# Performance work log

Measured on AMD Instinct MI355X. Metric: run time of the kernel, lower is better.

Reference implementation:

```python
import jax, jax.numpy as jnp
import numpy as np

B, C, H, W = 32, 3, 512, 512
OUT = (64, 64)  # (out_grid[0]=Nx, out_grid[1]=Ny)
SMALL = 1e-4


def setup_inputs() -> dict:
    key = jax.random.key(0)
    k1, k2 = jax.random.split(key, 2)
    X = jax.random.normal(k1, (B, C, H, W), dtype=jnp.float32)
    fan_in = C * H * W
    # localization net: flatten + dense(5); scaled so p ~ N(0,1) and exp(p) is stable
    W_loc = jax.random.normal(k2, (fan_in, 5), dtype=jnp.float32) / np.float32(np.sqrt(fan_in))
    b_loc = jnp.zeros((5,), dtype=jnp.float32)
    return {"X": X, "W_loc": W_loc, "b_loc": b_loc}


def reference(X, W_loc, b_loc):
    Bn = X.shape[0]
    # locnet: p = flatten(X) @ W_loc + b_loc  -> [B, 5]
    p = X.reshape(Bn, -1) @ W_loc + b_loc

    N = min(OUT)
    gx = OUT[0] * (p[:, 0] + 1.0) / 2.0          # [B]
    gy = OUT[1] * (p[:, 1] + 1.0) / 2.0          # [B]
    sigma2 = jnp.exp(p[:, 2])                    # [B]
    delta = jnp.exp(p[:, 3]) * (max(W, H) - 1) / (N - 1.0)  # [B]
    gamma = jnp.exp(p[:, 4])                     # [B]

    i1 = jnp.arange(OUT[0], dtype=jnp.float32)   # [Nx]
    i2 = jnp.arange(OUT[1], dtype=jnp.float32)   # [Ny]
    a = jnp.arange(W, dtype=jnp.float32)         # [W]
    b = jnp.arange(H, dtype=jnp.float32)         # [H]

    mx = gx[:, None] + delta[:, None] * (i1 - N / 2.0 - 0.5)  # [B, Nx]
    my = gy[:, None] + delta[:, None] * (i2 - N / 2.0 - 0.5)  # [B, Ny]

    Fx = jnp.exp(-((a - mx[:, :, None]) ** 2) / (2.0 * sigma2[:, None, None]))  # [B,Nx,W]
    Fx = Fx / (Fx.sum(axis=-1, keepdims=True) + SMALL)
    Fy = jnp.exp(-((b - my[:, :, None]) ** 2) / (2.0 * sigma2[:, None, None]))  # [B,Ny,H]
    Fy = Fy / (Fy.sum(axis=-1, keepdims=True) + SMALL)

    # glimpse read: gamma * Fy @ X @ Fx^T, done as batched contractions
    Fyx = jnp.einsum('bnh,bchw->bcnw', Fy, X)        # [B,C,Ny,W]
    out = jnp.einsum('bcnw,bmw->bcnm', Fyx, Fx)      # [B,C,Ny,Nx]
    return gamma[:, None, None, None] * out
```

## Files before the change

### kernel.cpp

```cpp
#include <hip/hip_runtime.h>
#include <math.h>

#define B_ 32
#define C_ 3
#define H_ 512
#define W_ 512
#define NOUT 64
#define FAN (C_*H_*W_)

#define CHUNKS 384
#define CELEMS (FAN / CHUNKS)
#define BGROUPS 4

#define P_OFF 0
#define FX_OFF 256
#define FY_OFF (FX_OFF + B_*NOUT*W_)

typedef __bf16 bf16x8 __attribute__((ext_vector_type(8)));
typedef float f32x4 __attribute__((ext_vector_type(4)));

__device__ __forceinline__ unsigned short f2bf(float f) {
    unsigned int u = __float_as_uint(f);
    u = (u + 0x7FFFu + ((u >> 16) & 1u)) >> 16;
    return (unsigned short)u;
}
__device__ __forceinline__ float bf2f(unsigned short h) {
    return __uint_as_float(((unsigned int)h) << 16);
}

__global__ __launch_bounds__(256) void k_locnet(const float* __restrict__ X,
                                                const float* __restrict__ Wl,
                                                float* __restrict__ ws) {
    const int chunk = blockIdx.x;
    const int b0 = blockIdx.y * 8;
    const int t = threadIdx.x;

    float acc[8][5] = {};
    const size_t base = (size_t)chunk * CELEMS;

    for (int k = t; k < CELEMS / 4; k += 256) {
        const size_t i0 = base + (size_t)k * 4;
        const float4* W4 = (const float4*)(Wl + i0 * 5);
        float4 w0 = W4[0], w1 = W4[1], w2 = W4[2], w3 = W4[3], w4 = W4[4];
        float wv[20] = {w0.x, w0.y, w0.z, w0.w,
                        w1.x, w1.y, w1.z, w1.w,
                        w2.x, w2.y, w2.z, w2.w,
                        w3.x, w3.y, w3.z, w3.w,
                        w4.x, w4.y, w4.z, w4.w};
        #pragma unroll
        for (int bb = 0; bb < 8; bb++) {
            float4 x = *(const float4*)(X + (size_t)(b0 + bb) * FAN + i0);
            float xv[4] = {x.x, x.y, x.z, x.w};
            #pragma unroll
            for (int e = 0; e < 4; e++)
                #pragma unroll
                for (int j = 0; j < 5; j++)
                    acc[bb][j] += xv[e] * wv[e * 5 + j];
        }
    }

    #pragma unroll
    for (int off = 32; off > 0; off >>= 1)
        #pragma unroll
        for (int bb = 0; bb < 8; bb++)
            #pragma unroll
            for (int j = 0; j < 5; j++)
                acc[bb][j] += __shfl_down(acc[bb][j], off);

    __shared__ float sred[4][40];
    const int wave = t >> 6, lane = t & 63;
    if (lane == 0) {
        #pragma unroll
        for (int bb = 0; bb < 8; bb++)
            #pragma unroll
            for (int j = 0; j < 5; j++)
                sred[wave][bb * 5 + j] = acc[bb][j];
    }
    __syncthreads();
    if (t < 40) {
        float s = sred[0][t] + sred[1][t] + sred[2][t] + sred[3][t];
        atomicAdd(&ws[P_OFF + b0 * 5 + t], s);
    }
}

__global__ __launch_bounds__(256) void k_filters(const float* __restrict__ bl,
                                                 float* __restrict__ ws) {
    const int n = blockIdx.x;
    const int b = blockIdx.y;
    const int which = blockIdx.z;
    const int t = threadIdx.x;

    const float p0 = ws[P_OFF + b * 5 + 0] + bl[0];
    const float p1 = ws[P_OFF + b * 5 + 1] + bl[1];
    const float p2 = ws[P_OFF + b * 5 + 2] + bl[2];
    const float p3 = ws[P_OFF + b * 5 + 3] + bl[3];

    const float g = (which == 0) ? 32.f * (p0 + 1.f) : 32.f * (p1 + 1.f);
    const float sigma2 = expf(p2);
    const float inv2s = 0.5f / sigma2;
    const float delta = expf(p3) * (511.0f / 63.0f);
    const float mean = g + delta * ((float)n - 32.5f);

    float d0 = (float)t - mean;
    float f0 = expf(-d0 * d0 * inv2s);
    float d1 = (float)(t + 256) - mean;
    float f1 = expf(-d1 * d1 * inv2s);

    float s = f0 + f1;
    #pragma unroll
    for (int off = 32; off > 0; off >>= 1) s += __shfl_down(s, off);
    __shared__ float sred[4];
    __shared__ float stot;
    const int wave = t >> 6, lane = t & 63;
    if (lane == 0) sred[wave] = s;
    __syncthreads();
    if (t == 0) stot = sred[0] + sred[1] + sred[2] + sred[3] + 1e-4f;
    __syncthreads();
    const float scale = 1.0f / stot;

    float* dst = ws + (which == 0 ? FX_OFF : FY_OFF) + ((size_t)b * NOUT + n) * W_;
    dst[t] = f0 * scale;
    dst[t + 256] = f1 * scale;
}

#define KC 64
#define PITCH 72
#define TSZ (64 * PITCH)

__global__ __launch_bounds__(256) void k_glimpse(const float* __restrict__ X,
                                                 const float* __restrict__ bl,
                                                 const float* __restrict__ ws,
                                                 float* __restrict__ out) {
    const int hc = blockIdx.x;
    const int bc = blockIdx.y;
    const int b = bc / 3;
    const int t = threadIdx.x;
    const int lane = t & 63;
    const int wv = t >> 6;
    const int l15 = lane & 15;
    const int quad = lane >> 4;
    const int hbase = hc * 64;

    __shared__ __align__(16) unsigned short lds[4 * TSZ];
    unsigned short* Xh = lds;
    unsigned short* Xl = lds + TSZ;
    unsigned short* Fh = lds + 2 * TSZ;
    unsigned short* Fl = lds + 3 * TSZ;

    const float* Xp  = X + (size_t)bc * (H_ * W_) + (size_t)hbase * W_;
    const float* Fxp = ws + FX_OFF + (size_t)b * NOUT * W_;
    const float* Fyp = ws + FY_OFF + (size_t)b * NOUT * W_;

    f32x4 acc[4] = {};

    for (int wt = 0; wt < 8; wt++) {
        const int wbase = wt * KC;
        #pragma unroll
        for (int k4 = 0; k4 < 4; k4++) {
            int idx = t + 256 * k4;
            int row = idx >> 4;
            int c4 = (idx & 15) * 4;
            float4 xv = *(const float4*)(Xp + (size_t)row * W_ + wbase + c4);
            float4 fv = *(const float4*)(Fxp + (size_t)row * W_ + wbase + c4);
            float xa[4] = {xv.x, xv.y, xv.z, xv.w};
            float fa[4] = {fv.x, fv.y, fv.z, fv.w};
            unsigned int xhp[2], xlp[2], fhp[2], flp[2];
            #pragma unroll
            for (int hwd = 0; hwd < 2; hwd++) {
                unsigned short h0 = f2bf(xa[2*hwd]);
                unsigned short h1 = f2bf(xa[2*hwd+1]);
                xhp[hwd] = (unsigned int)h0 | ((unsigned int)h1 << 16);
                unsigned short l0 = f2bf(xa[2*hwd] - bf2f(h0));
                unsigned short l1 = f2bf(xa[2*hwd+1] - bf2f(h1));
                xlp[hwd] = (unsigned int)l0 | ((unsigned int)l1 << 16);
                unsigned short g0 = f2bf(fa[2*hwd]);
                unsigned short g1 = f2bf(fa[2*hwd+1]);
                fhp[hwd] = (unsigned int)g0 | ((unsigned int)g1 << 16);
                unsigned short m0 = f2bf(fa[2*hwd] - bf2f(g0));
                unsigned short m1 = f2bf(fa[2*hwd+1] - bf2f(g1));
                flp[hwd] = (unsigned int)m0 | ((unsigned int)m1 << 16);
            }
            int o = row * PITCH + c4;
            *(uint2*)&Xh[o] = make_uint2(xhp[0], xhp[1]);
            *(uint2*)&Xl[o] = make_uint2(xlp[0], xlp[1]);
            *(uint2*)&Fh[o] = make_uint2(fhp[0], fhp[1]);
            *(uint2*)&Fl[o] = make_uint2(flp[0], flp[1]);
        }
        __syncthreads();
        #pragma unroll
        for (int ks = 0; ks < 2; ks++) {
            const int ko = ks * 32 + quad * 8;
            bf16x8 ah = *(const bf16x8*)&Xh[(16 * wv + l15) * PITCH + ko];
            bf16x8 al = *(const bf16x8*)&Xl[(16 * wv + l15) * PITCH + ko];
            #pragma unroll
            for (int mt = 0; mt < 4; mt++) {
                bf16x8 bh = *(const bf16x8*)&Fh[(16 * mt + l15) * PITCH + ko];
                bf16x8 bl2 = *(const bf16x8*)&Fl[(16 * mt + l15) * PITCH + ko];
                acc[mt] = __builtin_amdgcn_mfma_f32_16x16x32_bf16(ah, bh, acc[mt], 0, 0, 0);
                acc[mt] = __builtin_amdgcn_mfma_f32_16x16x32_bf16(al, bh, acc[mt], 0, 0, 0);
                acc[mt] = __builtin_amdgcn_mfma_f32_16x16x32_bf16(ah, bl2, acc[mt], 0, 0, 0);
            }
        }
        __syncthreads();
    }

    #pragma unroll
    for (int mt = 0; mt < 4; mt++) {
        unsigned int ghp[2], glp[2];
        unsigned short gh[4], gl[4];
        #pragma unroll
        for (int r = 0; r < 4; r++) {
            float g = acc[mt][r];
            gh[r] = f2bf(g);
            gl[r] = f2bf(g - bf2f(gh[r]));
        }
        ghp[0] = (unsigned int)gh[0] | ((unsigned int)gh[1] << 16);
        ghp[1] = (unsigned int)gh[2] | ((unsigned int)gh[3] << 16);
        glp[0] = (unsigned int)gl[0] | ((unsigned int)gl[1] << 16);
        glp[1] = (unsigned int)gl[2] | ((unsigned int)gl[3] << 16);
        int m = 16 * mt + l15;
        int h = 16 * wv + quad * 4;
        int o = m * PITCH + h;
        *(uint2*)&Xh[o] = make_uint2(ghp[0], ghp[1]);
        *(uint2*)&Xl[o] = make_uint2(glp[0], glp[1]);
    }

    #pragma unroll
    for (int k4 = 0; k4 < 4; k4++) {
        int idx = t + 256 * k4;
        int n = idx >> 4;
        int c4 = (idx & 15) * 4;
        float4 fv = *(const float4*)(Fyp + (size_t)n * W_ + hbase + c4);
        float fa[4] = {fv.x, fv.y, fv.z, fv.w};
        unsigned int fhp[2], flp[2];
        #pragma unroll
        for (int hwd = 0; hwd < 2; hwd++) {
            unsigned short g0 = f2bf(fa[2*hwd]);
            unsigned short g1 = f2bf(fa[2*hwd+1]);
            fhp[hwd] = (unsigned int)g0 | ((unsigned int)g1 << 16);
            unsigned short m0 = f2bf(fa[2*hwd] - bf2f(g0));
            unsigned short m1 = f2bf(fa[2*hwd+1] - bf2f(g1));
            flp[hwd] = (unsigned int)m0 | ((unsigned int)m1 << 16);
        }
        int o = n * PITCH + c4;
        *(uint2*)&Fh[o] = make_uint2(fhp[0], fhp[1]);
        *(uint2*)&Fl[o] = make_uint2(flp[0], flp[1]);
    }
    __syncthreads();

    f32x4 p[4] = {};
    #pragma unroll
    for (int ks = 0; ks < 2; ks++) {
        const int ko = ks * 32 + quad * 8;
        bf16x8 yh = *(const bf16x8*)&Fh[(16 * wv + l15) * PITCH + ko];
        bf16x8 yl = *(const bf16x8*)&Fl[(16 * wv + l15) * PITCH + ko];
        #pragma unroll
        for (int mt = 0; mt < 4; mt++) {
            bf16x8 gh = *(const bf16x8*)&Xh[(16 * mt + l15) * PITCH + ko];
            bf16x8 gl = *(const bf16x8*)&Xl[(16 * mt + l15) * PITCH + ko];
            p[mt] = __builtin_amdgcn_mfma_f32_16x16x32_bf16(yh, gh, p[mt], 0, 0, 0);
            p[mt] = __builtin_amdgcn_mfma_f32_16x16x32_bf16(yl, gh, p[mt], 0, 0, 0);
            p[mt] = __builtin_amdgcn_mfma_f32_16x16x32_bf16(yh, gl, p[mt], 0, 0, 0);
        }
    }

    const float gamma = expf(ws[P_OFF + b * 5 + 4] + bl[4]);
    float* outp = out + (size_t)bc * (NOUT * NOUT);
    #pragma unroll
    for (int mt = 0; mt < 4; mt++)
        #pragma unroll
        for (int r = 0; r < 4; r++) {
            int n = 16 * wv + quad * 4 + r;
            int m = 16 * mt + l15;
            atomicAdd(&outp[n * NOUT + m], gamma * p[mt][r]);
        }
}

extern "C" void kernel_launch(void* const* d_in, const int* in_sizes, int n_in,
                              void* d_out, int out_size, void* d_ws, size_t ws_size,
                              hipStream_t stream) {
    const float* X  = (const float*)d_in[0];
    const float* Wl = (const float*)d_in[1];
    const float* bl = (const float*)d_in[2];
    float* out = (float*)d_out;
    float* ws  = (float*)d_ws;

    hipMemsetAsync(ws, 0, 1024, stream);
    hipMemsetAsync(out, 0, (size_t)out_size * sizeof(float), stream);

    k_locnet<<<dim3(CHUNKS, BGROUPS), 256, 0, stream>>>(X, Wl, ws);
    k_filters<<<dim3(NOUT, B_, 2), 256, 0, stream>>>(bl, ws);
    k_glimpse<<<dim3(8, B_ * C_), 256, 0, stream>>>(X, bl, ws, out);
}
```

Measured before the change: 212.7 us.

## Precompute bf16 hi/lo filter splits, replicate locnet atomics, fold output zeroing

The filter kernel now stores Fx/Fy already split into bf16 hi and lo halves, so the glimpse kernel copies them straight into LDS with 16-byte loads instead of converting fp32 for every tile. X and intermediate conversions use the packed v_cvt_pk_bf16_f32 instruction. Locnet partial sums are spread across 8 replicas to reduce atomic contention, with half as many chunks. The output memset is replaced by zeroing inside the filter kernel. In exchange, readers must sum the 8 replicas, and the hardware conversion's rounding may differ slightly from the manual routine.

```diff
diff --git a/kernel.cpp b/kernel.cpp
--- a/kernel.cpp
+++ b/kernel.cpp
@@ -8,13 +8,16 @@
 #define NOUT 64
 #define FAN (C_*H_*W_)
 
-#define CHUNKS 384
+#define CHUNKS 192
 #define CELEMS (FAN / CHUNKS)
 #define BGROUPS 4
-
-#define P_OFF 0
-#define FX_OFF 256
-#define FY_OFF (FX_OFF + B_*NOUT*W_)
+#define NREP 8
+
+#define PFLOATS 2048
+#define FXH_U 0
+#define FXL_U 1048576
+#define FYH_U 2097152
+#define FYL_U 3145728
 
 typedef __bf16 bf16x8 __attribute__((ext_vector_type(8)));
 typedef float f32x4 __attribute__((ext_vector_type(4)));
@@ -26,6 +29,11 @@
 }
 __device__ __forceinline__ float bf2f(unsigned short h) {
     return __uint_as_float(((unsigned int)h) << 16);
+}
+__device__ __forceinline__ unsigned int cvt_pk_bf16(float lo, float hi) {
+    unsigned int r;
+    asm("v_cvt_pk_bf16_f32 %0, %1, %2" : "=v"(r) : "v"(lo), "v"(hi));
+    return r;
 }
 
 __global__ __launch_bounds__(256) void k_locnet(const float* __restrict__ X,
@@ -34,6 +42,7 @@
     const int chunk = blockIdx.x;
     const int b0 = blockIdx.y * 8;
     const int t = threadIdx.x;
+    const int rep = chunk & (NREP - 1);
 
     float acc[8][5] = {};
     const size_t base = (size_t)chunk * CELEMS;
@@ -79,21 +88,32 @@
     __syncthreads();
     if (t < 40) {
         float s = sred[0][t] + sred[1][t] + sred[2][t] + sred[3][t];
-        atomicAdd(&ws[P_OFF + b0 * 5 + t], s);
+        atomicAdd(&ws[rep * 256 + b0 * 5 + t], s);
     }
 }
 
 __global__ __launch_bounds__(256) void k_filters(const float* __restrict__ bl,
-                                                 float* __restrict__ ws) {
+                                                 float* __restrict__ ws,
+                                                 float* __restrict__ out) {
     const int n = blockIdx.x;
     const int b = blockIdx.y;
     const int which = blockIdx.z;
     const int t = threadIdx.x;
 
-    const float p0 = ws[P_OFF + b * 5 + 0] + bl[0];
-    const float p1 = ws[P_OFF + b * 5 + 1] + bl[1];
-    const float p2 = ws[P_OFF + b * 5 + 2] + bl[2];
-    const float p3 = ws[P_OFF + b * 5 + 3] + bl[3];
+    {
+        const int bid = blockIdx.x + NOUT * (blockIdx.y + B_ * blockIdx.z);
+        if (t < 24) {
+            float4 z = make_float4(0.f, 0.f, 0.f, 0.f);
+            ((float4*)out)[(size_t)bid * 24 + t] = z;
+        }
+    }
+
+    float p0 = bl[0], p1 = bl[1], p2 = bl[2], p3 = bl[3];
+    #pragma unroll
+    for (int rep = 0; rep < NREP; rep++) {
+        const float* pr = ws + rep * 256 + b * 5;
+        p0 += pr[0]; p1 += pr[1]; p2 += pr[2]; p3 += pr[3];
+    }
 
     const float g = (which == 0) ? 32.f * (p0 + 1.f) : 32.f * (p1 + 1.f);
     const float sigma2 = expf(p2);
@@ -118,9 +138,18 @@
     __syncthreads();
     const float scale = 1.0f / stot;
 
-    float* dst = ws + (which == 0 ? FX_OFF : FY_OFF) + ((size_t)b * NOUT + n) * W_;
-    dst[t] = f0 * scale;
-    dst[t + 256] = f1 * scale;
+    unsigned short* wsu = (unsigned short*)(ws + PFLOATS);
+    unsigned short* dstH = wsu + (which ? FYH_U : FXH_U) + ((size_t)b * NOUT + n) * 512;
+    unsigned short* dstL = wsu + (which ? FYL_U : FXL_U) + ((size_t)b * NOUT + n) * 512;
+
+    float v0 = f0 * scale;
+    unsigned short h0 = f2bf(v0);
+    dstH[t] = h0;
+    dstL[t] = f2bf(v0 - bf2f(h0));
+    float v1 = f1 * scale;
+    unsigned short h1 = f2bf(v1);
+    dstH[t + 256] = h1;
+    dstL[t + 256] = f2bf(v1 - bf2f(h1));
 }
 
 #define KC 64
@@ -147,9 +176,12 @@
     unsigned short* Fh = lds + 2 * TSZ;
     unsigned short* Fl = lds + 3 * TSZ;
 
-    const float* Xp  = X + (size_t)bc * (H_ * W_) + (size_t)hbase * W_;
-    const float* Fxp = ws + FX_OFF + (size_t)b * NOUT * W_;
-    const float* Fyp = ws + FY_OFF + (size_t)b * NOUT * W_;
+    const float* Xp = X + (size_t)bc * (H_ * W_) + (size_t)hbase * W_;
+    const unsigned short* wsu = (const unsigned short*)(ws + PFLOATS);
+    const unsigned short* FxHp = wsu + FXH_U + (size_t)b * NOUT * 512;
+    const unsigned short* FxLp = wsu + FXL_U + (size_t)b * NOUT * 512;
+    const unsigned short* FyHp = wsu + FYH_U + (size_t)b * NOUT * 512;
+    const unsigned short* FyLp = wsu + FYL_U + (size_t)b * NOUT * 512;
 
     f32x4 acc[4] = {};
 
@@ -161,30 +193,27 @@
             int row = idx >> 4;
             int c4 = (idx & 15) * 4;
             float4 xv = *(const float4*)(Xp + (size_t)row * W_ + wbase + c4);
-            float4 fv = *(const float4*)(Fxp + (size_t)row * W_ + wbase + c4);
-            float xa[4] = {xv.x, xv.y, xv.z, xv.w};
-            float fa[4] = {fv.x, fv.y, fv.z, fv.w};
-            unsigned int xhp[2], xlp[2], fhp[2], flp[2];
-            #pragma unroll
-            for (int hwd = 0; hwd < 2; hwd++) {
-                unsigned short h0 = f2bf(xa[2*hwd]);
-                unsigned short h1 = f2bf(xa[2*hwd+1]);
-                xhp[hwd] = (unsigned int)h0 | ((unsigned int)h1 << 16);
-                unsigned short l0 = f2bf(xa[2*hwd] - bf2f(h0));
-                unsigned short l1 = f2bf(xa[2*hwd+1] - bf2f(h1));
-                xlp[hwd] = (unsigned int)l0 | ((unsigned int)l1 << 16);
-                unsigned short g0 = f2bf(fa[2*hwd]);
-                unsigned short g1 = f2bf(fa[2*hwd+1]);
-                fhp[hwd] = (unsigned int)g0 | ((unsigned int)g1 << 16);
-                unsigned short m0 = f2bf(fa[2*hwd] - bf2f(g0));
-                unsigned short m1 = f2bf(fa[2*hwd+1] - bf2f(g1));
-                flp[hwd] = (unsigned int)m0 | ((unsigned int)m1 << 16);
-            }
+            unsigned int h01 = cvt_pk_bf16(xv.x, xv.y);
+            unsigned int h23 = cvt_pk_bf16(xv.z, xv.w);
+            float r0 = __uint_as_float(h01 << 16);
+            float r1 = __uint_as_float(h01 & 0xffff0000u);
+            float r2 = __uint_as_float(h23 << 16);
+            float r3 = __uint_as_float(h23 & 0xffff0000u);
+            unsigned int l01 = cvt_pk_bf16(xv.x - r0, xv.y - r1);
+            unsigned int l23 = cvt_pk_bf16(xv.z - r2, xv.w - r3);
             int o = row * PITCH + c4;
-            *(uint2*)&Xh[o] = make_uint2(xhp[0], xhp[1]);
-            *(uint2*)&Xl[o] = make_uint2(xlp[0], xlp[1]);
-            *(uint2*)&Fh[o] = make_uint2(fhp[0], fhp[1]);
-            *(uint2*)&Fl[o] = make_uint2(flp[0], flp[1]);
+            *(uint2*)&Xh[o] = make_uint2(h01, h23);
+            *(uint2*)&Xl[o] = make_uint2(l01, l23);
+        }
+        #pragma unroll
+        for (int i = 0; i < 2; i++) {
+            int idx = t + 256 * i;
+            int row = idx >> 3;
+            int c8 = (idx & 7) * 8;
+            uint4 hv = *(const uint4*)(FxHp + (size_t)row * 512 + wbase + c8);
+            uint4 lv = *(const uint4*)(FxLp + (size_t)row * 512 + wbase + c8);
+            *(uint4*)&Fh[row * PITCH + c8] = hv;
+            *(uint4*)&Fl[row * PITCH + c8] = lv;
         }
         __syncthreads();
         #pragma unroll
@@ -206,45 +235,31 @@
 
     #pragma unroll
     for (int mt = 0; mt < 4; mt++) {
-        unsigned int ghp[2], glp[2];
-        unsigned short gh[4], gl[4];
-        #pragma unroll
-        for (int r = 0; r < 4; r++) {
-            float g = acc[mt][r];
-            gh[r] = f2bf(g);
-            gl[r] = f2bf(g - bf2f(gh[r]));
-        }
-        ghp[0] = (unsigned int)gh[0] | ((unsigned int)gh[1] << 16);
-        ghp[1] = (unsigned int)gh[2] | ((unsigned int)gh[3] << 16);
-        glp[0] = (unsigned int)gl[0] | ((unsigned int)gl[1] << 16);
-        glp[1] = (unsigned int)gl[2] | ((unsigned int)gl[3] << 16);
+        float g0 = acc[mt][0], g1 = acc[mt][1], g2 = acc[mt][2], g3 = acc[mt][3];
+        unsigned int h01 = cvt_pk_bf16(g0, g1);
+        unsigned int h23 = cvt_pk_bf16(g2, g3);
+        float r0 = __uint_as_float(h01 << 16);
+        float r1 = __uint_as_float(h01 & 0xffff0000u);
+        float r2 = __uint_as_float(h23 << 16);
+        float r3 = __uint_as_float(h23 & 0xffff0000u);
+        unsigned int l01 = cvt_pk_bf16(g0 - r0, g1 - r1);
+        unsigned int l23 = cvt_pk_bf16(g2 - r2, g3 - r3);
         int m = 16 * mt + l15;
         int h = 16 * wv + quad * 4;
         int o = m * PITCH + h;
-        *(uint2*)&Xh[o] = make_uint2(ghp[0], ghp[1]);
-        *(uint2*)&Xl[o] = make_uint2(glp[0], glp[1]);
-    }
-
-    #pragma unroll
-    for (int k4 = 0; k4 < 4; k4++) {
-        int idx = t + 256 * k4;
-        int n = idx >> 4;
-        int c4 = (idx & 15) * 4;
-        float4 fv = *(const float4*)(Fyp + (size_t)n * W_ + hbase + c4);
-        float fa[4] = {fv.x, fv.y, fv.z, fv.w};
-        unsigned int fhp[2], flp[2];
-        #pragma unroll
-        for (int hwd = 0; hwd < 2; hwd++) {
-            unsigned short g0 = f2bf(fa[2*hwd]);
-            unsigned short g1 = f2bf(fa[2*hwd+1]);
-            fhp[hwd] = (unsigned int)g0 | ((unsigned int)g1 << 16);
-            unsigned short m0 = f2bf(fa[2*hwd] - bf2f(g0));
-            unsigned short m1 = f2bf(fa[2*hwd+1] - bf2f(g1));
-            flp[hwd] = (unsigned int)m0 | ((unsigned int)m1 << 16);
-        }
-        int o = n * PITCH + c4;
-        *(uint2*)&Fh[o] = make_uint2(fhp[0], fhp[1]);
-        *(uint2*)&Fl[o] = make_uint2(flp[0], flp[1]);
+        *(uint2*)&Xh[o] = make_uint2(h01, h23);
+        *(uint2*)&Xl[o] = make_uint2(l01, l23);
+    }
+
+    #pragma unroll
+    for (int i = 0; i < 2; i++) {
+        int idx = t + 256 * i;
+        int row = idx >> 3;
+        int c8 = (idx & 7) * 8;
+        uint4 hv = *(const uint4*)(FyHp + (size_t)row * 512 + hbase + c8);
+        uint4 lv = *(const uint4*)(FyLp + (size_t)row * 512 + hbase + c8);
+        *(uint4*)&Fh[row * PITCH + c8] = hv;
+        *(uint4*)&Fl[row * PITCH + c8] = lv;
     }
     __syncthreads();
 
@@ -264,7 +279,11 @@
         }
     }
 
-    const float gamma = expf(ws[P_OFF + b * 5 + 4] + bl[4]);
+    float p4 = bl[4];
+    #pragma unroll
+    for (int rep = 0; rep < NREP; rep++) p4 += ws[rep * 256 + b * 5 + 4];
+    const float gamma = expf(p4);
+
     float* outp = out + (size_t)bc * (NOUT * NOUT);
     #pragma unroll
     for (int mt = 0; mt < 4; mt++)
@@ -285,10 +304,9 @@
     float* out = (float*)d_out;
     float* ws  = (float*)d_ws;
 
-    hipMemsetAsync(ws, 0, 1024, stream);
-    hipMemsetAsync(out, 0, (size_t)out_size * sizeof(float), stream);
+    hipMemsetAsync(ws, 0, PFLOATS * sizeof(float), stream);
 
     k_locnet<<<dim3(CHUNKS, BGROUPS), 256, 0, stream>>>(X, Wl, ws);
-    k_filters<<<dim3(NOUT, B_, 2), 256, 0, stream>>>(bl, ws);
+    k_filters<<<dim3(NOUT, B_, 2), 256, 0, stream>>>(bl, ws, out);
     k_glimpse<<<dim3(8, B_ * C_), 256, 0, stream>>>(X, bl, ws, out);
 }
```

Result: faster. 205.6 us (-3.3%).
